# Kernel optimization log

Hardware: AMD Instinct MI355X
Metric: run time of the kernel (lower is better)

## Reference

```python
import jax, jax.numpy as jnp
import numpy as np

B, S, H = 1, 2048, 2048
NH, KVH, HD = 32, 8, 64
N_REP = NH // KVH
SCALING = HD ** -0.5
NEG = -1e9  # large negative for causal additive mask


def rotate_half(x):
    x1, x2 = x[..., : HD // 2], x[..., HD // 2:]
    return jnp.concatenate((-x2, x1), axis=-1)


def setup_inputs() -> dict:
    key = jax.random.key(0)
    ks = jax.random.split(key, 6)
    hidden_states = jax.random.normal(ks[0], (B, S, H), dtype=jnp.float32)
    # RoPE tables, Llama style: freqs duplicated across both halves of head_dim
    inv_freq = 1.0 / (10000.0 ** (np.arange(0, HD, 2, dtype=np.float32) / HD))
    t = np.arange(S, dtype=np.float32)
    freqs = np.outer(t, inv_freq)              # [S, HD/2]
    emb = np.concatenate([freqs, freqs], -1)   # [S, HD]
    cos = jnp.asarray(np.cos(emb))[None]       # [1, S, HD]
    sin = jnp.asarray(np.sin(emb))[None]
    # additive causal mask [1,1,S,S]
    causal = jnp.where(jnp.tril(jnp.ones((S, S), bool)), 0.0, NEG).astype(jnp.float32)
    attention_mask = causal[None, None]
    std = 0.02
    Wq = jax.random.normal(ks[1], (NH * HD, H), dtype=jnp.float32) * std
    Wk = jax.random.normal(ks[2], (KVH * HD, H), dtype=jnp.float32) * std
    Wv = jax.random.normal(ks[3], (KVH * HD, H), dtype=jnp.float32) * std
    Wo = jax.random.normal(ks[4], (H, NH * HD), dtype=jnp.float32) * std
    return {"hidden_states": hidden_states, "cos": cos, "sin": sin,
            "attention_mask": attention_mask, "Wq": Wq, "Wk": Wk, "Wv": Wv, "Wo": Wo}


def reference(hidden_states, cos, sin, attention_mask, Wq, Wk, Wv, Wo):
    b, s, _ = hidden_states.shape
    # QKV projections -> [b, heads, s, hd]
    q = (hidden_states @ Wq.T).reshape(b, s, NH, HD).transpose(0, 2, 1, 3)
    k = (hidden_states @ Wk.T).reshape(b, s, KVH, HD).transpose(0, 2, 1, 3)
    v = (hidden_states @ Wv.T).reshape(b, s, KVH, HD).transpose(0, 2, 1, 3)
    # RoPE (cos/sin broadcast over heads via unsqueeze_dim=1)
    c, sn = cos[:, None], sin[:, None]  # [1,1,s,hd]
    q = q * c + rotate_half(q) * sn
    k = k * c + rotate_half(k) * sn
    # GQA repeat_kv (repeat_interleave over head dim)
    k = jnp.repeat(k, N_REP, axis=1)
    v = jnp.repeat(v, N_REP, axis=1)
    # eager attention with explicit [b,h,s,s] score matrix (fp32 softmax)
    scores = jnp.einsum('bhqd,bhkd->bhqk', q, k) * SCALING + attention_mask
    attn_weights = jax.nn.softmax(scores.astype(jnp.float32), axis=-1).astype(q.dtype)
    attn = jnp.einsum('bhqk,bhkd->bhqd', attn_weights, v)
    attn = attn.transpose(0, 2, 1, 3).reshape(b, s, NH * HD)
    out = attn @ Wo.T
    return out, attn_weights
```

## Files before the change

### kernel.cpp

```cpp
#include <hip/hip_runtime.h>
#include <hip/hip_bf16.h>
#include <type_traits>

#define S_LEN 2048
#define HDIM  2048
#define NHEADS 32
#define KVHEADS 8
#define HD 64
#define SCALE 0.125f

typedef __bf16 bf16;
typedef bf16  bf16x8 __attribute__((ext_vector_type(8)));
typedef float f32x4  __attribute__((ext_vector_type(4)));

__device__ __forceinline__ void gload16(const void* g, void* l) {
  __builtin_amdgcn_global_load_lds((const __attribute__((address_space(1))) void*)g,
                                   (__attribute__((address_space(3))) void*)l, 16, 0, 0);
}

template<int RB>
__device__ __forceinline__ bf16x8 frag_ld(const bf16* lds, int row, int kByte, int lane) {
  const char* p = reinterpret_cast<const char*>(lds) + row*RB
                + ((kByte + ((lane>>4)<<4)) ^ ((row&7)<<4));
  return *reinterpret_cast<const bf16x8*>(p);
}

__device__ __forceinline__ f32x4 mfma16(bf16x8 a, bf16x8 b, f32x4 c) {
  return __builtin_amdgcn_mfma_f32_16x16x32_bf16(a, b, c, 0, 0, 0);
}

__global__ void cvt_all(const float* __restrict__ hs, const float* __restrict__ wq,
                        const float* __restrict__ wk, const float* __restrict__ wv,
                        const float* __restrict__ wo, bf16* __restrict__ dst) {
  size_t c = (size_t)blockIdx.x*256 + threadIdx.x;
  const float* src;
  if      (c <  524288u)  src = hs + c*8;
  else if (c < 1048576u)  src = wq + (c - 524288u)*8;
  else if (c < 1179648u)  src = wk + (c - 1048576u)*8;
  else if (c < 1310720u)  src = wv + (c - 1179648u)*8;
  else                    src = wo + (c - 1310720u)*8;
  float4 a = *reinterpret_cast<const float4*>(src);
  float4 b = *reinterpret_cast<const float4*>(src + 4);
  bf16x8 o;
  o[0]=(bf16)a.x; o[1]=(bf16)a.y; o[2]=(bf16)a.z; o[3]=(bf16)a.w;
  o[4]=(bf16)b.x; o[5]=(bf16)b.y; o[6]=(bf16)b.z; o[7]=(bf16)b.w;
  *reinterpret_cast<bf16x8*>(dst + c*8) = o;
}

enum { EPI_QKV = 0, EPI_OUT = 2 };

template<int EPI>
__global__ __launch_bounds__(256) void gemm_bt(
    const bf16* __restrict__ A, const bf16* __restrict__ Bw,
    void* __restrict__ C0, void* __restrict__ C1, void* __restrict__ C2,
    const float* __restrict__ cosp, const float* __restrict__ sinp,
    int N, int K)
{
  __shared__ __align__(16) bf16 ls[3][2][128*64];
  const int t = threadIdx.x, lane = t & 63;
  const int w = t >> 6, wm = w & 1, wn = w >> 1;
  const int bm = blockIdx.x, bn = blockIdx.y;
  const int r8 = t >> 3, c8 = t & 7;
  const int llo = lane & 15, lhi = lane >> 4;
  const int nkt = K >> 6;

  auto stage = [&](int kt, int b) {
    #pragma unroll
    for (int i = 0; i < 4; i++) {
      int row = i*32 + r8;
      int chunk = c8 ^ (row & 7);
      gload16(A + (size_t)(bm*128 + row)*K + kt*64 + chunk*8,
              (char*)(&ls[b][0][0]) + i*4096 + t*16);
    }
    #pragma unroll
    for (int i = 0; i < 4; i++) {
      int row = i*32 + r8;
      int chunk = c8 ^ (row & 7);
      gload16(Bw + (size_t)(bn*128 + row)*K + kt*64 + chunk*8,
              (char*)(&ls[b][1][0]) + i*4096 + t*16);
    }
  };

  f32x4 acc[4][4] = {};
  stage(0, 0);
  stage(1, 1);
  int cur = 0;
  for (int kt = 0; kt < nkt; ++kt) {
    if (kt + 2 < nkt) {
      int nb = cur + 2; if (nb >= 3) nb -= 3;
      stage(kt + 2, nb);
      asm volatile("s_waitcnt vmcnt(16)" ::: "memory");
    } else if (kt + 1 < nkt) {
      asm volatile("s_waitcnt vmcnt(8)" ::: "memory");
    } else {
      asm volatile("s_waitcnt vmcnt(0)" ::: "memory");
    }
    __builtin_amdgcn_s_barrier();
    asm volatile("" ::: "memory");
    const bf16* lA = &ls[cur][0][0];
    const bf16* lB = &ls[cur][1][0];
    #pragma unroll
    for (int ks = 0; ks < 2; ++ks) {
      bf16x8 av[4], bv[4];
      #pragma unroll
      for (int m = 0; m < 4; m++) av[m] = frag_ld<128>(lA, wm*64 + m*16 + llo, ks*64, lane);
      #pragma unroll
      for (int n = 0; n < 4; n++) bv[n] = frag_ld<128>(lB, wn*64 + n*16 + llo, ks*64, lane);
      #pragma unroll
      for (int m = 0; m < 4; m++)
        #pragma unroll
        for (int n = 0; n < 4; n++)
          acc[m][n] = mfma16(av[m], bv[n], acc[m][n]);
    }
    asm volatile("s_waitcnt lgkmcnt(0)" ::: "memory");
    __builtin_amdgcn_s_barrier();
    if (++cur == 3) cur = 0;
  }

  const int rowb = bm*128 + wm*64 + lhi*4;
  const int colb = bn*128 + wn*64;
  if constexpr (EPI == EPI_OUT) {
    float* C = (float*)C0;
    #pragma unroll
    for (int m = 0; m < 4; m++)
      #pragma unroll
      for (int n = 0; n < 4; n++)
        #pragma unroll
        for (int r = 0; r < 4; r++) {
          int row = rowb + m*16 + r;
          int col = colb + n*16 + llo;
          C[(size_t)row*HDIM + col] = acc[m][n][r];
        }
  } else {
    #pragma unroll
    for (int m = 0; m < 4; m++)
      #pragma unroll
      for (int r = 0; r < 4; r++) {
        int row = rowb + m*16 + r;
        #pragma unroll
        for (int n = 0; n < 4; n++) {
          int col = colb + n*16 + llo;
          float v = acc[m][n][r];
          if (col < 2560) {
            float pr  = acc[m][n^2][r];
            float rot = (n & 2) ? pr : -pr;
            int d = col & 63;
            float cv = cosp[(size_t)row*HD + d];
            float sv = sinp[(size_t)row*HD + d];
            float o = v*cv + rot*sv;
            if (col < 2048) {
              int hh = col >> 6;
              ((bf16*)C0)[((size_t)hh*S_LEN + row)*HD + d] = (bf16)(o*SCALE);
            } else {
              int hh = (col - 2048) >> 6;
              ((bf16*)C1)[((size_t)hh*S_LEN + row)*HD + d] = (bf16)o;
            }
          } else {
            int c2 = col - 2560;
            int hh = c2 >> 6, d = c2 & 63;
            ((bf16*)C2)[((size_t)hh*HD + d)*S_LEN + row] = (bf16)v;
          }
        }
      }
  }
}

__global__ __launch_bounds__(256, 2) void attn_kernel(
    const bf16* __restrict__ qB, const bf16* __restrict__ kB, const bf16* __restrict__ vTB,
    float* __restrict__ attnw, bf16* __restrict__ aB)
{
  __shared__ __align__(16) bf16 lsP[128*128];
  __shared__ float lstat[256];
  const int t = threadIdx.x, lane = t & 63;
  const int w = t >> 6, wm = w & 1, wn = w >> 1;
  const int b = blockIdx.x;
  const int h = b >> 4;
  const int qraw = b & 15;
  const int qt = (b < 256) ? qraw : 15 - qraw;
  const int kvh = h >> 2;
  const int llo = lane & 15, lhi = lane >> 4;

  bf16x8 qa[4][2];
  #pragma unroll
  for (int m = 0; m < 4; m++)
    #pragma unroll
    for (int ks = 0; ks < 2; ks++)
      qa[m][ks] = *reinterpret_cast<const bf16x8*>(
        qB + ((size_t)h*S_LEN + qt*128 + wm*64 + m*16 + llo)*HD + ks*32 + lhi*8);

  float l_r[4][4];
  #pragma unroll
  for (int m = 0; m < 4; m++)
    #pragma unroll
    for (int r = 0; r < 4; r++) l_r[m][r] = 0.f;

  auto tileA = [&](int kt, auto diag_c) {
    constexpr bool DIAG = decltype(diag_c)::value;
    bf16x8 kb[4][2];
    #pragma unroll
    for (int n = 0; n < 4; n++)
      #pragma unroll
      for (int ks = 0; ks < 2; ks++)
        kb[n][ks] = *reinterpret_cast<const bf16x8*>(
          kB + ((size_t)kvh*S_LEN + kt*128 + wn*64 + n*16 + llo)*HD + ks*32 + lhi*8);
    f32x4 accs[4][4] = {};
    __builtin_amdgcn_s_setprio(1);
    #pragma unroll
    for (int ks = 0; ks < 2; ++ks)
      #pragma unroll
      for (int m = 0; m < 4; m++)
        #pragma unroll
        for (int n = 0; n < 4; n++) {
          if (DIAG && (wn*64 + n*16 > wm*64 + m*16 + 15)) continue;
          accs[m][n] = mfma16(qa[m][ks], kb[n][ks], accs[m][n]);
        }
    __builtin_amdgcn_s_setprio(0);
    #pragma unroll
    for (int m = 0; m < 4; m++) {
      #pragma unroll
      for (int r = 0; r < 4; r++) {
        float se = 0.f;
        if constexpr (DIAG) {
          int grow = qt*128 + wm*64 + m*16 + lhi*4 + r;
          #pragma unroll
          for (int n = 0; n < 4; n++) {
            int gcol = kt*128 + wn*64 + n*16 + llo;
            se += (gcol > grow) ? 0.f : __expf(accs[m][n][r]);
          }
        } else {
          #pragma unroll
          for (int n = 0; n < 4; n++) se += __expf(accs[m][n][r]);
        }
        #pragma unroll
        for (int off = 1; off < 16; off <<= 1) se += __shfl_xor(se, off);
        l_r[m][r] += se;
      }
    }
  };
  for (int kt = 0; kt < qt; ++kt) tileA(kt, std::false_type{});
  tileA(qt, std::true_type{});

  if (llo == 0) {
    #pragma unroll
    for (int m = 0; m < 4; m++)
      #pragma unroll
      for (int r = 0; r < 4; r++)
        lstat[wn*128 + wm*64 + m*16 + lhi*4 + r] = l_r[m][r];
  }
  __syncthreads();
  float linv[4][4];
  #pragma unroll
  for (int m = 0; m < 4; m++)
    #pragma unroll
    for (int r = 0; r < 4; r++) {
      int rg = wm*64 + m*16 + lhi*4 + r;
      linv[m][r] = 1.0f / (lstat[rg] + lstat[128 + rg]);
    }

  f32x4 acco[4][2] = {};
  float* awb = attnw + (size_t)h*S_LEN*S_LEN;

  auto tileB = [&](int kt, auto diag_c) {
    constexpr bool DIAG = decltype(diag_c)::value;
    bf16x8 kb[4][2];
    #pragma unroll
    for (int n = 0; n < 4; n++)
      #pragma unroll
      for (int ks = 0; ks < 2; ks++)
        kb[n][ks] = *reinterpret_cast<const bf16x8*>(
          kB + ((size_t)kvh*S_LEN + kt*128 + wn*64 + n*16 + llo)*HD + ks*32 + lhi*8);
    bf16x8 vb[2][4];
    #pragma unroll
    for (int n = 0; n < 2; n++)
      #pragma unroll
      for (int ks = 0; ks < 4; ks++)
        vb[n][ks] = *reinterpret_cast<const bf16x8*>(
          vTB + ((size_t)kvh*HD + wn*32 + n*16 + llo)*S_LEN + kt*128 + ks*32 + lhi*8);
    f32x4 accs[4][4] = {};
    __builtin_amdgcn_s_setprio(1);
    #pragma unroll
    for (int ks = 0; ks < 2; ++ks)
      #pragma unroll
      for (int m = 0; m < 4; m++)
        #pragma unroll
        for (int n = 0; n < 4; n++) {
          if (DIAG && (wn*64 + n*16 > wm*64 + m*16 + 15)) continue;
          accs[m][n] = mfma16(qa[m][ks], kb[n][ks], accs[m][n]);
        }
    __builtin_amdgcn_s_setprio(0);
    #pragma unroll
    for (int m = 0; m < 4; m++) {
      #pragma unroll
      for (int r = 0; r < 4; r++) {
        int rl = wm*64 + m*16 + lhi*4 + r;
        float li = linv[m][r];
        #pragma unroll
        for (int n = 0; n < 4; n++) {
          int cl = wn*64 + n*16 + llo;
          float p;
          if constexpr (DIAG) {
            int grow = qt*128 + rl;
            int gcol = kt*128 + cl;
            p = (gcol > grow) ? 0.f : __expf(accs[m][n][r])*li;
            if (gcol <= grow)
              __builtin_nontemporal_store(p, &awb[(size_t)grow*S_LEN + gcol]);
          } else {
            p = __expf(accs[m][n][r])*li;
            __builtin_nontemporal_store(p, &awb[(size_t)(qt*128 + rl)*S_LEN + kt*128 + cl]);
          }
          char* pp = (char*)lsP + rl*256 + ((cl*2) ^ ((rl & 7) << 4));
          *(bf16*)pp = (bf16)p;
        }
      }
    }
    asm volatile("s_waitcnt lgkmcnt(0)" ::: "memory");
    __builtin_amdgcn_s_barrier();
    asm volatile("" ::: "memory");
    __builtin_amdgcn_s_setprio(1);
    #pragma unroll
    for (int ks = 0; ks < 4; ++ks) {
      bf16x8 pa[4];
      #pragma unroll
      for (int m = 0; m < 4; m++) pa[m] = frag_ld<256>(lsP, wm*64 + m*16 + llo, ks*64, lane);
      #pragma unroll
      for (int m = 0; m < 4; m++)
        #pragma unroll
        for (int n = 0; n < 2; n++)
          acco[m][n] = mfma16(pa[m], vb[n][ks], acco[m][n]);
    }
    __builtin_amdgcn_s_setprio(0);
    asm volatile("s_waitcnt lgkmcnt(0)" ::: "memory");
    __builtin_amdgcn_s_barrier();
    asm volatile("" ::: "memory");
  };
  for (int kt = 0; kt < qt; ++kt) tileB(kt, std::false_type{});
  tileB(qt, std::true_type{});

  #pragma unroll
  for (int m = 0; m < 4; m++)
    #pragma unroll
    for (int n = 0; n < 2; n++)
      #pragma unroll
      for (int r = 0; r < 4; r++) {
        int grow = qt*128 + wm*64 + m*16 + lhi*4 + r;
        int gcol = h*HD + wn*32 + n*16 + llo;
        aB[(size_t)grow*HDIM + gcol] = (bf16)acco[m][n][r];
      }
}

extern "C" void kernel_launch(void* const* d_in, const int* in_sizes, int n_in,
                              void* d_out, int out_size, void* d_ws, size_t ws_size,
                              hipStream_t stream)
{
  (void)in_sizes; (void)n_in; (void)out_size; (void)ws_size;
  const float* hs   = (const float*)d_in[0];
  const float* cosp = (const float*)d_in[1];
  const float* sinp = (const float*)d_in[2];
  const float* Wq   = (const float*)d_in[4];
  const float* Wk   = (const float*)d_in[5];
  const float* Wv   = (const float*)d_in[6];
  const float* Wo   = (const float*)d_in[7];

  const size_t M4 = 4u*1024*1024, M1 = 1024u*1024;
  bf16* hsB = (bf16*)d_ws;
  bf16* WqB = hsB + M4;
  bf16* WkB = WqB + M4;
  bf16* WvB = WkB + M1;
  bf16* WoB = WvB + M1;
  bf16* qB  = WoB + M4;
  bf16* kB  = qB  + M4;
  bf16* vTB = kB  + M1;
  bf16* aB  = vTB + M1;

  float* outp  = (float*)d_out;
  float* attnw = outp + (size_t)S_LEN*HDIM;

  cvt_all<<<7168, 256, 0, stream>>>(hs, Wq, Wk, Wv, Wo, hsB);

  gemm_bt<EPI_QKV><<<dim3(16,24), 256, 0, stream>>>(hsB, WqB, qB, kB, vTB, cosp, sinp, 3072, 2048);
  attn_kernel<<<512, 256, 0, stream>>>(qB, kB, vTB, attnw, aB);
  gemm_bt<EPI_OUT><<<dim3(16,16), 256, 0, stream>>>(aB, WoB, outp, nullptr, nullptr,
                                                    nullptr, nullptr, 2048, 2048);
}
```

Measured before the change: 259.8 us.

## Coalesce attention-weight, V-transpose and output stores via LDS; shrink GEMM tiles

The attention kernel now writes attention weights as 16-byte vectorized, coalesced rows read back from the bf16 P tile in LDS, instead of scattered scalar fp32 stores. It also stages the per-head output through LDS before writing it to global memory. The row-sum shuffle reduction is moved out of the key-tile loop and done once. The projection GEMM moves from 128x128 triple-buffered tiles to 128x64 double-buffered tiles with two blocks per CU, and the V-transpose epilogue goes through LDS for coalesced writes. As a trade-off, the stored attention weights are now rounded to bf16 precision, and the smaller tiles reduce data reuse per block.

```diff
diff --git a/kernel.cpp b/kernel.cpp
--- a/kernel.cpp
+++ b/kernel.cpp
@@ -12,6 +12,7 @@
 typedef __bf16 bf16;
 typedef bf16  bf16x8 __attribute__((ext_vector_type(8)));
 typedef float f32x4  __attribute__((ext_vector_type(4)));
+typedef unsigned int u32;
 
 __device__ __forceinline__ void gload16(const void* g, void* l) {
   __builtin_amdgcn_global_load_lds((const __attribute__((address_space(1))) void*)g,
@@ -27,6 +28,18 @@
 
 __device__ __forceinline__ f32x4 mfma16(bf16x8 a, bf16x8 b, f32x4 c) {
   return __builtin_amdgcn_mfma_f32_16x16x32_bf16(a, b, c, 0, 0, 0);
+}
+
+__device__ __forceinline__ void bf8_to_f32(bf16x8 p, f32x4& lo, f32x4& hi) {
+  union { bf16x8 v; u32 d[4]; } u; u.v = p;
+  lo[0] = __builtin_bit_cast(float, u.d[0] << 16);
+  lo[1] = __builtin_bit_cast(float, u.d[0] & 0xffff0000u);
+  lo[2] = __builtin_bit_cast(float, u.d[1] << 16);
+  lo[3] = __builtin_bit_cast(float, u.d[1] & 0xffff0000u);
+  hi[0] = __builtin_bit_cast(float, u.d[2] << 16);
+  hi[1] = __builtin_bit_cast(float, u.d[2] & 0xffff0000u);
+  hi[2] = __builtin_bit_cast(float, u.d[3] << 16);
+  hi[3] = __builtin_bit_cast(float, u.d[3] & 0xffff0000u);
 }
 
 __global__ void cvt_all(const float* __restrict__ hs, const float* __restrict__ wq,
@@ -50,15 +63,16 @@
 enum { EPI_QKV = 0, EPI_OUT = 2 };
 
 template<int EPI>
-__global__ __launch_bounds__(256) void gemm_bt(
+__global__ __launch_bounds__(256, 2) void gemm_bt(
     const bf16* __restrict__ A, const bf16* __restrict__ Bw,
     void* __restrict__ C0, void* __restrict__ C1, void* __restrict__ C2,
     const float* __restrict__ cosp, const float* __restrict__ sinp,
     int N, int K)
 {
-  __shared__ __align__(16) bf16 ls[3][2][128*64];
+  __shared__ __align__(16) bf16 lsA[2][128*64];
+  __shared__ __align__(16) bf16 lsB[2][64*64];
   const int t = threadIdx.x, lane = t & 63;
-  const int w = t >> 6, wm = w & 1, wn = w >> 1;
+  const int w = t >> 6;
   const int bm = blockIdx.x, bn = blockIdx.y;
   const int r8 = t >> 3, c8 = t & 7;
   const int llo = lane & 15, lhi = lane >> 4;
@@ -70,98 +84,109 @@
       int row = i*32 + r8;
       int chunk = c8 ^ (row & 7);
       gload16(A + (size_t)(bm*128 + row)*K + kt*64 + chunk*8,
-              (char*)(&ls[b][0][0]) + i*4096 + t*16);
-    }
-    #pragma unroll
-    for (int i = 0; i < 4; i++) {
+              (char*)(&lsA[b][0]) + i*4096 + t*16);
+    }
+    #pragma unroll
+    for (int i = 0; i < 2; i++) {
       int row = i*32 + r8;
       int chunk = c8 ^ (row & 7);
-      gload16(Bw + (size_t)(bn*128 + row)*K + kt*64 + chunk*8,
-              (char*)(&ls[b][1][0]) + i*4096 + t*16);
+      gload16(Bw + (size_t)(bn*64 + row)*K + kt*64 + chunk*8,
+              (char*)(&lsB[b][0]) + i*4096 + t*16);
     }
   };
 
-  f32x4 acc[4][4] = {};
+  f32x4 acc[2][4] = {};
   stage(0, 0);
-  stage(1, 1);
-  int cur = 0;
   for (int kt = 0; kt < nkt; ++kt) {
-    if (kt + 2 < nkt) {
-      int nb = cur + 2; if (nb >= 3) nb -= 3;
-      stage(kt + 2, nb);
-      asm volatile("s_waitcnt vmcnt(16)" ::: "memory");
-    } else if (kt + 1 < nkt) {
-      asm volatile("s_waitcnt vmcnt(8)" ::: "memory");
+    if (kt + 1 < nkt) {
+      stage(kt + 1, (kt + 1) & 1);
+      asm volatile("s_waitcnt vmcnt(6)" ::: "memory");
     } else {
       asm volatile("s_waitcnt vmcnt(0)" ::: "memory");
     }
     __builtin_amdgcn_s_barrier();
     asm volatile("" ::: "memory");
-    const bf16* lA = &ls[cur][0][0];
-    const bf16* lB = &ls[cur][1][0];
+    const bf16* lA = &lsA[kt & 1][0];
+    const bf16* lB = &lsB[kt & 1][0];
     #pragma unroll
     for (int ks = 0; ks < 2; ++ks) {
-      bf16x8 av[4], bv[4];
-      #pragma unroll
-      for (int m = 0; m < 4; m++) av[m] = frag_ld<128>(lA, wm*64 + m*16 + llo, ks*64, lane);
-      #pragma unroll
-      for (int n = 0; n < 4; n++) bv[n] = frag_ld<128>(lB, wn*64 + n*16 + llo, ks*64, lane);
-      #pragma unroll
-      for (int m = 0; m < 4; m++)
+      bf16x8 av[2], bv[4];
+      #pragma unroll
+      for (int m = 0; m < 2; m++) av[m] = frag_ld<128>(lA, w*32 + m*16 + llo, ks*64, lane);
+      #pragma unroll
+      for (int n = 0; n < 4; n++) bv[n] = frag_ld<128>(lB, n*16 + llo, ks*64, lane);
+      #pragma unroll
+      for (int m = 0; m < 2; m++)
         #pragma unroll
         for (int n = 0; n < 4; n++)
           acc[m][n] = mfma16(av[m], bv[n], acc[m][n]);
     }
     asm volatile("s_waitcnt lgkmcnt(0)" ::: "memory");
     __builtin_amdgcn_s_barrier();
-    if (++cur == 3) cur = 0;
+    asm volatile("" ::: "memory");
   }
 
-  const int rowb = bm*128 + wm*64 + lhi*4;
-  const int colb = bn*128 + wn*64;
+  const int rowb = bm*128 + w*32 + lhi*4;
+  const int colb = bn*64;
   if constexpr (EPI == EPI_OUT) {
     float* C = (float*)C0;
     #pragma unroll
-    for (int m = 0; m < 4; m++)
+    for (int m = 0; m < 2; m++)
       #pragma unroll
       for (int n = 0; n < 4; n++)
         #pragma unroll
         for (int r = 0; r < 4; r++) {
           int row = rowb + m*16 + r;
           int col = colb + n*16 + llo;
-          C[(size_t)row*HDIM + col] = acc[m][n][r];
+          __builtin_nontemporal_store(acc[m][n][r], &C[(size_t)row*HDIM + col]);
         }
   } else {
-    #pragma unroll
-    for (int m = 0; m < 4; m++)
-      #pragma unroll
-      for (int r = 0; r < 4; r++) {
-        int row = rowb + m*16 + r;
-        #pragma unroll
-        for (int n = 0; n < 4; n++) {
-          int col = colb + n*16 + llo;
-          float v = acc[m][n][r];
-          if (col < 2560) {
-            float pr  = acc[m][n^2][r];
+    if (bn < 40) {
+      #pragma unroll
+      for (int m = 0; m < 2; m++)
+        #pragma unroll
+        for (int r = 0; r < 4; r++) {
+          int row = rowb + m*16 + r;
+          #pragma unroll
+          for (int n = 0; n < 4; n++) {
+            int d = n*16 + llo;
+            float v  = acc[m][n][r];
+            float pr = acc[m][n^2][r];
             float rot = (n & 2) ? pr : -pr;
-            int d = col & 63;
             float cv = cosp[(size_t)row*HD + d];
             float sv = sinp[(size_t)row*HD + d];
             float o = v*cv + rot*sv;
-            if (col < 2048) {
-              int hh = col >> 6;
-              ((bf16*)C0)[((size_t)hh*S_LEN + row)*HD + d] = (bf16)(o*SCALE);
+            if (bn < 32) {
+              ((bf16*)C0)[((size_t)bn*S_LEN + row)*HD + d] = (bf16)(o*SCALE);
             } else {
-              int hh = (col - 2048) >> 6;
-              ((bf16*)C1)[((size_t)hh*S_LEN + row)*HD + d] = (bf16)o;
+              ((bf16*)C1)[((size_t)(bn-32)*S_LEN + row)*HD + d] = (bf16)o;
             }
-          } else {
-            int c2 = col - 2560;
-            int hh = c2 >> 6, d = c2 & 63;
-            ((bf16*)C2)[((size_t)hh*HD + d)*S_LEN + row] = (bf16)v;
           }
         }
+    } else {
+      bf16* lsT = &lsA[0][0];
+      #pragma unroll
+      for (int m = 0; m < 2; m++)
+        #pragma unroll
+        for (int n = 0; n < 4; n++)
+          #pragma unroll
+          for (int r = 0; r < 4; r++) {
+            int d  = n*16 + llo;
+            int sl = w*32 + m*16 + lhi*4 + r;
+            char* pp = (char*)lsT + d*256 + ((sl*2) ^ ((d & 7) << 4));
+            *(bf16*)pp = (bf16)acc[m][n][r];
+          }
+      __syncthreads();
+      bf16* vT = (bf16*)C2;
+      #pragma unroll
+      for (int i = 0; i < 4; i++) {
+        int rid = i*16 + (t >> 4);
+        int c   = t & 15;
+        bf16x8 v = *(const bf16x8*)((char*)lsT + rid*256 + ((c*16) ^ ((rid & 7) << 4)));
+        *reinterpret_cast<bf16x8*>(
+          vT + ((size_t)(bn-40)*HD + rid)*S_LEN + bm*128 + c*8) = v;
       }
+    }
   }
 }
 
@@ -219,27 +244,32 @@
     for (int m = 0; m < 4; m++) {
       #pragma unroll
       for (int r = 0; r < 4; r++) {
-        float se = 0.f;
         if constexpr (DIAG) {
           int grow = qt*128 + wm*64 + m*16 + lhi*4 + r;
           #pragma unroll
           for (int n = 0; n < 4; n++) {
             int gcol = kt*128 + wn*64 + n*16 + llo;
-            se += (gcol > grow) ? 0.f : __expf(accs[m][n][r]);
+            l_r[m][r] += (gcol > grow) ? 0.f : __expf(accs[m][n][r]);
           }
         } else {
           #pragma unroll
-          for (int n = 0; n < 4; n++) se += __expf(accs[m][n][r]);
-        }
-        #pragma unroll
-        for (int off = 1; off < 16; off <<= 1) se += __shfl_xor(se, off);
-        l_r[m][r] += se;
+          for (int n = 0; n < 4; n++) l_r[m][r] += __expf(accs[m][n][r]);
+        }
       }
     }
   };
   for (int kt = 0; kt < qt; ++kt) tileA(kt, std::false_type{});
   tileA(qt, std::true_type{});
 
+  #pragma unroll
+  for (int m = 0; m < 4; m++)
+    #pragma unroll
+    for (int r = 0; r < 4; r++) {
+      float se = l_r[m][r];
+      #pragma unroll
+      for (int off = 1; off < 16; off <<= 1) se += __shfl_xor(se, off);
+      l_r[m][r] = se;
+    }
   if (llo == 0) {
     #pragma unroll
     for (int m = 0; m < 4; m++)
@@ -302,11 +332,8 @@
             int grow = qt*128 + rl;
             int gcol = kt*128 + cl;
             p = (gcol > grow) ? 0.f : __expf(accs[m][n][r])*li;
-            if (gcol <= grow)
-              __builtin_nontemporal_store(p, &awb[(size_t)grow*S_LEN + gcol]);
           } else {
             p = __expf(accs[m][n][r])*li;
-            __builtin_nontemporal_store(p, &awb[(size_t)(qt*128 + rl)*S_LEN + kt*128 + cl]);
           }
           char* pp = (char*)lsP + rl*256 + ((cl*2) ^ ((rl & 7) << 4));
           *(bf16*)pp = (bf16)p;
@@ -329,6 +356,21 @@
           acco[m][n] = mfma16(pa[m], vb[n][ks], acco[m][n]);
     }
     __builtin_amdgcn_s_setprio(0);
+    #pragma unroll
+    for (int i = 0; i < 4; i++) {
+      int rl = i*32 + (t >> 3);
+      int c2 = (t & 7)*2;
+      bf16x8 p0 = *(const bf16x8*)((char*)lsP + rl*256 + ((c2*16)     ^ ((rl & 7) << 4)));
+      bf16x8 p1 = *(const bf16x8*)((char*)lsP + rl*256 + (((c2+1)*16) ^ ((rl & 7) << 4)));
+      f32x4 f0, f1, f2, f3;
+      bf8_to_f32(p0, f0, f1);
+      bf8_to_f32(p1, f2, f3);
+      float* dst = awb + (size_t)(qt*128 + rl)*S_LEN + kt*128 + c2*8;
+      __builtin_nontemporal_store(f0, (f32x4*)(dst));
+      __builtin_nontemporal_store(f1, (f32x4*)(dst + 4));
+      __builtin_nontemporal_store(f2, (f32x4*)(dst + 8));
+      __builtin_nontemporal_store(f3, (f32x4*)(dst + 12));
+    }
     asm volatile("s_waitcnt lgkmcnt(0)" ::: "memory");
     __builtin_amdgcn_s_barrier();
     asm volatile("" ::: "memory");
@@ -342,10 +384,19 @@
     for (int n = 0; n < 2; n++)
       #pragma unroll
       for (int r = 0; r < 4; r++) {
-        int grow = qt*128 + wm*64 + m*16 + lhi*4 + r;
-        int gcol = h*HD + wn*32 + n*16 + llo;
-        aB[(size_t)grow*HDIM + gcol] = (bf16)acco[m][n][r];
+        int rl = wm*64 + m*16 + lhi*4 + r;
+        int cl = wn*32 + n*16 + llo;
+        char* pp = (char*)lsP + rl*128 + ((cl*2) ^ ((rl & 7) << 4));
+        *(bf16*)pp = (bf16)acco[m][n][r];
       }
+  __syncthreads();
+  #pragma unroll
+  for (int i = 0; i < 4; i++) {
+    int rl = i*32 + (t >> 3);
+    int c  = t & 7;
+    bf16x8 v = *(const bf16x8*)((char*)lsP + rl*128 + ((c*16) ^ ((rl & 7) << 4)));
+    *reinterpret_cast<bf16x8*>(aB + (size_t)(qt*128 + rl)*HDIM + h*HD + c*8) = v;
+  }
 }
 
 extern "C" void kernel_launch(void* const* d_in, const int* in_sizes, int n_in,
@@ -377,8 +428,8 @@
 
   cvt_all<<<7168, 256, 0, stream>>>(hs, Wq, Wk, Wv, Wo, hsB);
 
-  gemm_bt<EPI_QKV><<<dim3(16,24), 256, 0, stream>>>(hsB, WqB, qB, kB, vTB, cosp, sinp, 3072, 2048);
+  gemm_bt<EPI_QKV><<<dim3(16,48), 256, 0, stream>>>(hsB, WqB, qB, kB, vTB, cosp, sinp, 3072, 2048);
   attn_kernel<<<512, 256, 0, stream>>>(qB, kB, vTB, attnw, aB);
-  gemm_bt<EPI_OUT><<<dim3(16,16), 256, 0, stream>>>(aB, WoB, outp, nullptr, nullptr,
+  gemm_bt<EPI_OUT><<<dim3(16,32), 256, 0, stream>>>(aB, WoB, outp, nullptr, nullptr,
                                                     nullptr, nullptr, 2048, 2048);
 }
```

New measurement: 432.4 us. 66.4% more time.
